# Performance work log

Hardware: AMD Instinct MI355X
Metric: run time of the kernel (lower is better)

## Reference

```python
import math
import jax, jax.numpy as jnp
import numpy as np

NPIX = 262144  # 512x512 flattened pixel map


def _shift_matrix(kmax):
    """Faithful numpy port of EPG.EPG_shift_matrices (incl. the S[0:2,4]=1 quirk)."""
    N = 3 * (kmax + 1)
    Sf = np.zeros((N * N,), dtype=np.complex64)
    kidx = list(range(3, N, 3))
    sidx = [x - 3 for x in kidx]
    Sf[[a + N * b for a, b in zip(kidx, sidx)]] = 1
    kidx = list(range(4, N, 3))[:-1]
    sidx = [x + 3 for x in kidx]
    Sf[[a + N * b for a, b in zip(kidx, sidx)]] = 1
    kidx = list(range(2, N, 3))
    Sf[[a + N * a for a in kidx]] = 1
    S = Sf.reshape(N, N).T.copy()
    S[0:2, 4] = 1
    return S


def _rf_rot(alpha, phi):
    """Faithful numpy port of EPG.RF_rot (complex 3x3 RF rotation)."""
    cos2 = np.cos(alpha / 2.0) ** 2
    sin2 = np.sin(alpha / 2.0) ** 2
    sina = np.sin(alpha)
    cosa = np.cos(alpha)
    r10 = np.exp(-2j * phi) * sin2
    RR = np.array([
        [cos2, np.conj(r10), -1j * np.exp(1j * phi) * sina],
        [r10, cos2, 1j * np.exp(-1j * phi) * sina],
        [-0.5j * np.exp(-1j * phi) * sina, 0.5j * np.exp(1j * phi) * sina, cosa],
    ], dtype=np.complex64)
    return RR


def setup_inputs() -> dict:
    key = jax.random.key(0)
    qm = jax.random.uniform(key, (1, 3, NPIX, 1), dtype=jnp.float32)
    return {"quantitative_maps": qm, "n_pulses": 32, "TR": 15}


def reference(quantitative_maps, n_pulses, TR):
    # forward(): PD/T1/T2 maps, each [npix, 1]
    PD = quantitative_maps[0, 0, :, :]
    T1 = quantitative_maps[0, 1, :, :] * 5000.0 + 0.01
    T2 = quantitative_maps[0, 2, :, :] * 1500.0 + 0.01
    TRf = jnp.float32(TR)

    # EPG_GRE static setup (kmax_per_pulse cap logic from the source)
    np2 = int(n_pulses)
    kpp = list(range(1, math.ceil(np2 / 2) + 1)) + list(range(math.floor(np2 / 2), 0, -1))
    kmax = min(np2 - 1, max(kpp))
    K = kmax + 1
    N = 3 * K  # EPG state width (F+, F-, Z per k-order)

    S = jnp.asarray(_shift_matrix(kmax))  # [N, N] complex64, gradient shift
    # theta = 0.25*pi for every pulse (forward hardcodes this) -> A constant
    A = jnp.asarray(_rf_rot(0.25 * np.pi, 0.0))  # [3, 3] complex64

    E1 = jnp.exp(-TRf / T1)[:, 0]  # [npix]
    E2 = jnp.exp(-TRf / T2)[:, 0]  # [npix]
    # E = kron(I_K, diag(E2, E2, E1)) is diagonal -> keep only the diagonal vector
    Evec = jnp.tile(jnp.stack([E2, E2, E1], axis=1), (1, K)).astype(jnp.complex64)  # [npix, N]
    b = jnp.zeros((E1.shape[0], N), jnp.complex64).at[:, 2].set(1.0 - E1)

    FF0 = jnp.zeros((E1.shape[0], N), jnp.complex64).at[:, 2].set(1.0)

    def step(FF, _):
        # T = kron(I_K, A): apply A to each 3-block of the state
        Fj = jnp.einsum('ij,pkj->pki', A, FF.reshape(-1, K, 3)).reshape(FF.shape)  # [npix, N]
        # relaxation + shift + recovery, then conjugation (as in EPG_GRE loop)
        FF_next = jnp.conj(Evec * (Fj @ S.T) + b)
        return FF_next, Fj[:, 0]  # echo = F+0 state after RF pulse

    _, echoes = jax.lax.scan(step, FF0, None, length=np2)  # [np2, npix]
    s = echoes.T  # [npix, np2] == F[:, 0, :]
    return jnp.abs(s) * PD  # PD [npix,1] broadcasts -> [npix, np2]
```

## Files before the change

kernel.cpp:

```cpp
#include <hip/hip_runtime.h>
#include <math.h>
#include <utility>


#define NPULSES 32
#define KMAX 17

__host__ __device__ constexpr int cmin3(int a, int b, int c) {
    int m = a < b ? a : b; return m < c ? m : c;
}

template <typename F, int... Ts>
__device__ __forceinline__ void static_for(F&& f, std::integer_sequence<int, Ts...>) {
    (f(std::integral_constant<int, Ts>{}), ...);
}

__global__ __launch_bounds__(256) void epg_kernel(
    const float* __restrict__ qm,
    const int* __restrict__ tr_ptr,
    float* __restrict__ out,
    int npix)
{
    __shared__ float lds[256 * 33];
    const int tid = threadIdx.x;
    const int p = blockIdx.x * 256 + tid;
    const bool valid = (p < npix);

    float PD = valid ? qm[p] : 0.0f;
    float T1 = valid ? fmaf(qm[npix + p], 5000.0f, 0.01f) : 1.0f;
    float T2 = valid ? fmaf(qm[2 * npix + p], 1500.0f, 0.01f) : 1.0f;
    float TR = (float)(*tr_ptr);
    float E1 = __expf(-TR / T1);
    float E2 = __expf(-TR / T2);

    const float c2 = 0.8535533905932737f;
    const float s2 = 0.1464466094067263f;
    const float sa = 0.7071067811865476f;

    float Aa = -E2 * c2;
    float Bb = -E2 * s2;
    float C  =  E2 * sa;
    float D  =  E1 * 0.5f * sa;
    float Ez =  E1 * sa;
    float inj = (1.0f - E1) * PD;

    float fp[KMAX], fm[KMAX - 1], z[KMAX - 1];
    #pragma unroll
    for (int k = 0; k < KMAX; ++k) fp[k] = 0.0f;
    #pragma unroll
    for (int k = 0; k < KMAX - 1; ++k) { fm[k] = 0.0f; z[k] = 0.0f; }
    z[0] = PD;

    static_for([&](auto tc) {
        constexpr int t = decltype(tc)::value;
        constexpr int A = cmin3(t, KMAX, (NPULSES - 1) - t);

        float e = fmaf(c2, fp[0], fmaf(s2, fm[0], -sa * z[0]));
        lds[tid * 33 + t] = fabsf(e);

        if constexpr (t < NPULSES - 1) {
            float rm_prev = 0.0f;
            static_for([&](auto jc) {
                constexpr int j = A - decltype(jc)::value;
                float pk = fp[j], mk = fm[j], zk = z[j];
                float Cz = C * zk;
                float rp = fmaf(Aa, pk, fmaf(Bb, mk,  Cz));
                float rm = fmaf(Bb, pk, fmaf(Aa, mk, -Cz));
                float zn = fmaf(Ez, zk, D * (pk - mk));
                fp[j + 1] = rp;
                fm[j] = rm_prev;
                z[j] = zn;
                rm_prev = rm;
            }, std::make_integer_sequence<int, A + 1>{});
            fp[0] = fm[0];
            z[0] += inj;
        }
    }, std::make_integer_sequence<int, NPULSES>{});

    __syncthreads();

    const int l = tid & 63;
    const int w = tid >> 6;
    float4* dst = (float4*)(out + ((size_t)blockIdx.x * 256 + w * 64) * NPULSES);
    const int wave_pix_base = blockIdx.x * 256 + w * 64;
    if (wave_pix_base + 64 <= npix) {
        #pragma unroll
        for (int i = 0; i < 8; ++i) {
            int q  = i * 8 + (l >> 3);
            int t0 = (l & 7) * 4;
            const float* s = &lds[(w * 64 + q) * 33 + t0];
            dst[i * 64 + l] = make_float4(s[0], s[1], s[2], s[3]);
        }
    }
}

extern "C" void kernel_launch(void* const* d_in, const int* in_sizes, int n_in,
                              void* d_out, int out_size, void* d_ws, size_t ws_size,
                              hipStream_t stream) {
    const float* qm = (const float*)d_in[0];
    const int* tr = (const int*)d_in[2];
    float* out = (float*)d_out;
    int npix = in_sizes[0] / 3;

    int block = 256;
    int grid = (npix + block - 1) / block;
    epg_kernel<<<grid, block, 0, stream>>>(qm, tr, out, npix);
}
```

Baseline: 21.13 us.

## Process two pixels per thread with packed float2 FMA and direct stores

Each thread now handles two pixels using 2-wide float vectors, so the compiler can emit packed FP32 FMA instructions for the EPG recurrence. The LDS transpose buffer and barrier are removed, and each thread writes its echoes straight to global memory as float4 stores every four pulses. State arrays are trimmed to 16 slots because higher orders never feed the echo. In exchange, register pressure roughly doubles, the grid halves, and the per-pixel strided float4 stores are less coalesced than the previous staged writes.

```diff
diff --git a/kernel.cpp b/kernel.cpp
--- a/kernel.cpp
+++ b/kernel.cpp
@@ -5,6 +5,9 @@
 
 #define NPULSES 32
 #define KMAX 17
+#define NSLOT 16
+
+typedef float v2f __attribute__((ext_vector_type(2)));
 
 __host__ __device__ constexpr int cmin3(int a, int b, int c) {
     int m = a < b ? a : b; return m < c ? m : c;
@@ -15,83 +18,86 @@
     (f(std::integral_constant<int, Ts>{}), ...);
 }
 
+__device__ __forceinline__ v2f fma2(v2f a, v2f b, v2f c) {
+    return __builtin_elementwise_fma(a, b, c);
+}
+
 __global__ __launch_bounds__(256) void epg_kernel(
     const float* __restrict__ qm,
     const int* __restrict__ tr_ptr,
     float* __restrict__ out,
     int npix)
 {
-    __shared__ float lds[256 * 33];
     const int tid = threadIdx.x;
-    const int p = blockIdx.x * 256 + tid;
-    const bool valid = (p < npix);
+    const int l = tid & 63, w = tid >> 6;
+    const int pixA = blockIdx.x * 512 + w * 128 + l;
+    if (pixA >= npix) return;
+    const bool hasB = (pixA + 64) < npix;
+    const int pixB = hasB ? pixA + 64 : pixA;
 
-    float PD = valid ? qm[p] : 0.0f;
-    float T1 = valid ? fmaf(qm[npix + p], 5000.0f, 0.01f) : 1.0f;
-    float T2 = valid ? fmaf(qm[2 * npix + p], 1500.0f, 0.01f) : 1.0f;
     float TR = (float)(*tr_ptr);
-    float E1 = __expf(-TR / T1);
-    float E2 = __expf(-TR / T2);
+
+    v2f PD  = { qm[pixA], qm[pixB] };
+    v2f T1  = { fmaf(qm[npix + pixA], 5000.0f, 0.01f),
+                fmaf(qm[npix + pixB], 5000.0f, 0.01f) };
+    v2f T2v = { fmaf(qm[2 * npix + pixA], 1500.0f, 0.01f),
+                fmaf(qm[2 * npix + pixB], 1500.0f, 0.01f) };
+    v2f E1  = { __expf(-TR / T1.x),  __expf(-TR / T1.y)  };
+    v2f E2  = { __expf(-TR / T2v.x), __expf(-TR / T2v.y) };
 
     const float c2 = 0.8535533905932737f;
     const float s2 = 0.1464466094067263f;
     const float sa = 0.7071067811865476f;
+    const v2f C2v = { c2, c2 }, S2v = { s2, s2 }, SAv = { sa, sa };
 
-    float Aa = -E2 * c2;
-    float Bb = -E2 * s2;
-    float C  =  E2 * sa;
-    float D  =  E1 * 0.5f * sa;
-    float Ez =  E1 * sa;
-    float inj = (1.0f - E1) * PD;
+    v2f Aa  = -c2 * E2;
+    v2f Bb  = -s2 * E2;
+    v2f Cc  =  sa * E2;
+    v2f Dd  = (0.5f * sa) * E1;
+    v2f Ez  =  sa * E1;
+    v2f inj = (1.0f - E1) * PD;
 
-    float fp[KMAX], fm[KMAX - 1], z[KMAX - 1];
-    #pragma unroll
-    for (int k = 0; k < KMAX; ++k) fp[k] = 0.0f;
-    #pragma unroll
-    for (int k = 0; k < KMAX - 1; ++k) { fm[k] = 0.0f; z[k] = 0.0f; }
+    v2f fp[NSLOT], fm[NSLOT], z[NSLOT];
+    static_for([&](auto kc) {
+        constexpr int k = decltype(kc)::value;
+        fp[k] = (v2f){0.0f, 0.0f}; fm[k] = (v2f){0.0f, 0.0f}; z[k] = (v2f){0.0f, 0.0f};
+    }, std::make_integer_sequence<int, NSLOT>{});
     z[0] = PD;
+
+    float4* oA = (float4*)(out + (size_t)pixA * NPULSES);
+    float4* oB = (float4*)(out + (size_t)pixB * NPULSES);
+    v2f ebuf[4];
 
     static_for([&](auto tc) {
         constexpr int t = decltype(tc)::value;
-        constexpr int A = cmin3(t, KMAX, (NPULSES - 1) - t);
 
-        float e = fmaf(c2, fp[0], fmaf(s2, fm[0], -sa * z[0]));
-        lds[tid * 33 + t] = fabsf(e);
+        v2f e = fma2(C2v, fp[0], fma2(S2v, fm[0], -(SAv * z[0])));
+        ebuf[t & 3] = __builtin_elementwise_abs(e);
+        if constexpr ((t & 3) == 3) {
+            oA[t >> 2] = make_float4(ebuf[0].x, ebuf[1].x, ebuf[2].x, ebuf[3].x);
+            if (hasB)
+                oB[t >> 2] = make_float4(ebuf[0].y, ebuf[1].y, ebuf[2].y, ebuf[3].y);
+        }
 
         if constexpr (t < NPULSES - 1) {
-            float rm_prev = 0.0f;
+            constexpr int A = cmin3(t, KMAX, (NPULSES - 1) - t);
+            v2f rm_prev = (v2f){0.0f, 0.0f};
             static_for([&](auto jc) {
                 constexpr int j = A - decltype(jc)::value;
-                float pk = fp[j], mk = fm[j], zk = z[j];
-                float Cz = C * zk;
-                float rp = fmaf(Aa, pk, fmaf(Bb, mk,  Cz));
-                float rm = fmaf(Bb, pk, fmaf(Aa, mk, -Cz));
-                float zn = fmaf(Ez, zk, D * (pk - mk));
-                fp[j + 1] = rp;
+                v2f pk = fp[j], mk = fm[j], zk = z[j];
+                v2f Cz = Cc * zk;
+                v2f rp = fma2(Aa, pk, fma2(Bb, mk,  Cz));
+                v2f rm = fma2(Bb, pk, fma2(Aa, mk, -Cz));
+                v2f zn = fma2(Ez, zk, Dd * (pk - mk));
+                if constexpr (j < NSLOT - 1) fp[j + 1] = rp;
                 fm[j] = rm_prev;
-                z[j] = zn;
+                z[j]  = zn;
                 rm_prev = rm;
             }, std::make_integer_sequence<int, A + 1>{});
             fp[0] = fm[0];
             z[0] += inj;
         }
     }, std::make_integer_sequence<int, NPULSES>{});
-
-    __syncthreads();
-
-    const int l = tid & 63;
-    const int w = tid >> 6;
-    float4* dst = (float4*)(out + ((size_t)blockIdx.x * 256 + w * 64) * NPULSES);
-    const int wave_pix_base = blockIdx.x * 256 + w * 64;
-    if (wave_pix_base + 64 <= npix) {
-        #pragma unroll
-        for (int i = 0; i < 8; ++i) {
-            int q  = i * 8 + (l >> 3);
-            int t0 = (l & 7) * 4;
-            const float* s = &lds[(w * 64 + q) * 33 + t0];
-            dst[i * 64 + l] = make_float4(s[0], s[1], s[2], s[3]);
-        }
-    }
 }
 
 extern "C" void kernel_launch(void* const* d_in, const int* in_sizes, int n_in,
@@ -103,6 +109,6 @@
     int npix = in_sizes[0] / 3;
 
     int block = 256;
-    int grid = (npix + block - 1) / block;
+    int grid = (npix + 511) / 512;
     epg_kernel<<<grid, block, 0, stream>>>(qm, tr, out, npix);
 }
```

Measured after the change: 36.41 us. +72.3%, slower.
